# Kernel tuning notes

Measured on AMD Instinct MI355X. Metric: run time of the kernel, lower is better.

Reference implementation:

```python
import jax, jax.numpy as jnp
import numpy as np

EPS = 1e-3  # tfa InstanceNormalization default epsilon


def _inorm(x, g, b):
    # instance norm over the last two axes (the spatial extent of the attention map)
    mu = jnp.mean(x, axis=(-2, -1), keepdims=True)
    var = jnp.var(x, axis=(-2, -1), keepdims=True)
    return (x - mu) * jax.lax.rsqrt(var + EPS) * g + b


def setup_inputs() -> dict:
    key = jax.random.key(0)
    B, N, E, H = 4, 576, 256, 8
    C = 4 * E  # KV_size
    ks = jax.random.split(key, 24)

    def w(k, i, o):
        return jax.random.normal(k, (i, o), jnp.float32) * 0.02

    return {
        "emb1": jax.random.normal(ks[0], (B, N, E), jnp.float32),
        "emb2": jax.random.normal(ks[1], (B, N, E), jnp.float32),
        "emb3": jax.random.normal(ks[2], (B, N, E), jnp.float32),
        "emb4": jax.random.normal(ks[3], (B, N, E), jnp.float32),
        "emb_C": jax.random.normal(ks[4], (B, N, C), jnp.float32),
        "Wq_C": w(ks[5], C, C),
        "Wk_C": w(ks[6], C, C),
        "Wv_C": w(ks[7], C, C),
        "Wq1": w(ks[8], E, E),
        "Wq2": w(ks[9], E, E),
        "Wq3": w(ks[10], E, E),
        "Wq4": w(ks[11], E, E),
        "Wk": w(ks[12], E, E),
        "Wv": w(ks[13], E, E),
        "Wo1": w(ks[14], E, E),
        "Wo2": w(ks[15], E, E),
        "Wo3": w(ks[16], E, E),
        "Wo4": w(ks[17], E, E),
        "gamma1": jnp.ones((), jnp.float32),   # psi1 scale (channel axis has size 1)
        "beta1": jnp.zeros((), jnp.float32),
        "gamma2": jnp.ones((H,), jnp.float32),  # psi2 scale, channel axis = heads
        "beta2": jnp.zeros((H,), jnp.float32),
    }


def reference(emb1, emb2, emb3, emb4, emb_C, Wq_C, Wk_C, Wv_C,
              Wq1, Wq2, Wq3, Wq4, Wk, Wv, Wo1, Wo2, Wo3, Wo4,
              gamma1, beta1, gamma2, beta2):
    B, N, E = emb1.shape
    H = gamma2.shape[0]
    dh = E // H

    # ---- channel attention (inline InstanceNorm + softmax) ----
    QC = emb_C @ Wq_C  # (B,N,C)
    KC = emb_C @ Wk_C
    VC = emb_C @ Wv_C
    attn_c = jnp.einsum('bnc,bnd->bcd', QC, KC)                    # (B,C,C)
    sim_c = jax.nn.softmax(_inorm(attn_c, gamma1, beta1), axis=-1)
    T_hat = jnp.einsum('bcd,bnd->bnc', sim_c, VC)                  # (B,N,C)

    # split channel dim (C = 4E) into 4 chunks of E, concat along tokens -> (B,4N,E)
    KV_S = jnp.transpose(T_hat.reshape(B, N, 4, E), (0, 2, 1, 3)).reshape(B, 4 * N, E)

    def heads(x):  # (B,L,E) -> (B,H,L,dh)
        L = x.shape[1]
        return jnp.transpose(x.reshape(B, L, H, dh), (0, 2, 1, 3))

    # ---- 4-branch spatial multi-head attention with shared K/V ----
    Qs = jnp.stack([heads(emb1 @ Wq1), heads(emb2 @ Wq2),
                    heads(emb3 @ Wq3), heads(emb4 @ Wq4)])          # (4,B,H,N,dh)
    Kh = heads(KV_S @ Wk)                                           # (B,H,4N,dh)
    Vh = heads(KV_S @ Wv)

    attn = jnp.einsum('qbhnd,bhmd->qbhnm', Qs, Kh)                  # (4,B,H,N,4N)
    g = gamma2[:, None, None]
    b = beta2[:, None, None]
    sim = jax.nn.softmax(_inorm(attn, g, b), axis=-1)
    ctx = jnp.einsum('qbhnm,bhmd->qbhnd', sim, Vh)                  # (4,B,H,N,dh)
    ctx = jnp.transpose(ctx, (0, 1, 3, 2, 4)).reshape(4, B, N, E)

    return (ctx[0] @ Wo1, ctx[1] @ Wo2, ctx[2] @ Wo3, ctx[3] @ Wo4)
```

## Files before the change

### kernel.cpp

```cpp
#include <hip/hip_runtime.h>
#include <math.h>


namespace {
constexpr int Bq  = 4;
constexpr int Nn  = 576;
constexpr int Ee  = 256;
constexpr int Cc  = 1024;
constexpr int Mm  = 2304;
constexpr long BNE = (long)Bq * Nn * Ee;
constexpr long CCl = (long)Cc * Cc;
constexpr float EPSV = 1e-3f;
constexpr float LOG2E = 1.4426950408889634f;
}

typedef _Float16 h16;
typedef _Float16 h8v __attribute__((ext_vector_type(8)));
typedef _Float16 h4v __attribute__((ext_vector_type(4)));
typedef float    f4v __attribute__((ext_vector_type(4)));

struct WtP {
  const float* src[13]; h16* dst[13];
  const float* embC; h16* dEmbC;
};

__global__ __launch_bounds__(256) void wtrans(WtP p)
{
  const int bt = blockIdx.x;
  const int t = threadIdx.x;
  if (bt >= 928) {
    const long i4 = ((long)(bt - 928) * 256 + t) * 4;
    const float4 v = *(const float4*)(p.embC + i4);
    h4v o = {(h16)v.x, (h16)v.y, (h16)v.z, (h16)v.w};
    *(h4v*)(p.dEmbC + i4) = o;
    return;
  }
  __shared__ h16 Ls[64][64];
  int mi, tile, Kd, Nd;
  if (bt < 768) { mi = bt >> 8; tile = bt & 255; Kd = 1024; Nd = 1024; }
  else { const int r = bt - 768; mi = 3 + (r >> 4); tile = r & 15; Kd = 256; Nd = 256; }
  const int ntn = Nd >> 6;
  const int tk = tile / ntn, tn = tile % ntn;
  const float* src = p.src[mi] + (long)(tk * 64) * Nd + tn * 64;
  h16* dst = p.dst[mi] + (long)(tn * 64) * Kd + tk * 64;
  #pragma unroll
  for (int it = 0; it < 4; ++it) {
    const int kr = (t >> 4) + it * 16;
    const int c4 = (t & 15) * 4;
    const float4 v = *(const float4*)(src + (long)kr * Nd + c4);
    const float vv[4] = {v.x, v.y, v.z, v.w};
    #pragma unroll
    for (int jj = 0; jj < 4; ++jj) {
      const int n = c4 + jj;
      Ls[n][(((kr >> 3) ^ ((n >> 3) & 7)) << 3) | (kr & 7)] = (h16)vv[jj];
    }
  }
  __syncthreads();
  #pragma unroll
  for (int it = 0; it < 2; ++it) {
    const int n = t >> 2;
    const int k8 = (t & 3) + it * 4;
    const h8v o = *(const h8v*)&Ls[n][(k8 ^ ((n >> 3) & 7)) << 3];
    *(h8v*)(dst + (long)n * Kd + k8 * 8) = o;
  }
}

__global__ __launch_bounds__(256) void vtrans(
    const h16* __restrict__ V, h16* __restrict__ vT)
{
  __shared__ h16 Ls[32][64];
  const int kc = blockIdx.x;
  const int bh = blockIdx.y;
  const int b = bh >> 3, h = bh & 7;
  const int t = threadIdx.x;
  const int kv0 = kc * 64;
  {
    const int row = t >> 2, c8 = t & 3;
    const h8v v = *(const h8v*)(V + ((long)b * Mm + kv0 + row) * Ee + h * 32 + c8 * 8);
    #pragma unroll
    for (int e = 0; e < 8; ++e) {
      const int d = c8 * 8 + e;
      Ls[d][(((row >> 3) ^ ((d >> 3) & 7)) << 3) | (row & 7)] = v[e];
    }
  }
  __syncthreads();
  {
    const int d = t >> 3, j8 = t & 7;
    const h8v o = *(const h8v*)&Ls[d][(j8 ^ ((d >> 3) & 7)) << 3];
    *(h8v*)(vT + ((long)bh * 32 + d) * Mm + kv0 + j8 * 8) = o;
  }
}

struct GemmP {
  const h16* A[4]; const h16* B[4]; void* O[4][3]; const float* A32[4];
};

template <int BM, int TA, int TB, int AF32, int OUT16, int RM, int STATS, int OSHIFT>
__global__ __launch_bounds__(256) void mg(GemmP p, int K, int lda, int ldb,
                                          int ldc, float* stats)
{
  __shared__ h16 As[BM][64];
  __shared__ h16 Bs[128][64];
  const int z = blockIdx.z;
  const h16* A = p.A[z]; const h16* B = p.B[z]; const float* A32 = p.A32[z];
  const int n0 = blockIdx.x * 128, m0 = blockIdx.y * BM;
  const int t = threadIdx.x, w = t >> 6, lg = (t >> 4) & 3, lr = t & 15;
  constexpr int MF = 4, NF = (BM == 128 ? 4 : 2);
  const int wm = (BM == 128) ? (w & 1) * 64 : 0;
  const int wn = (BM == 128) ? (w >> 1) * 64 : w * 32;

  h8v   rA[AF32 ? 1 : BM / 32];
  float4 rF[AF32 ? BM / 16 : 1];
  h8v   rB[4];

  auto LOAD = [&](int kt) {
    if constexpr (AF32) {
      #pragma unroll
      for (int it = 0; it < BM / 16; ++it) {
        const int f = t + it * 256, row = f >> 4, c4 = f & 15;
        rF[it] = *(const float4*)(A32 + (long)(m0 + row) * lda + kt + c4 * 4);
      }
    } else if constexpr (TA == 0) {
      #pragma unroll
      for (int it = 0; it < BM / 32; ++it) {
        const int f = t + it * 256, row = f >> 3, c8 = f & 7;
        rA[it] = *(const h8v*)(A + (long)(m0 + row) * lda + kt + c8 * 8);
      }
    } else {
      #pragma unroll
      for (int it = 0; it < BM / 32; ++it) {
        const int f = t + it * 256;
        const int kr = (BM == 128) ? (f >> 4) : (f >> 3);
        const int mc = (BM == 128) ? (f & 15) : (f & 7);
        rA[it] = *(const h8v*)(A + (long)(kt + kr) * lda + m0 + mc * 8);
      }
    }
    if constexpr (TB == 0) {
      #pragma unroll
      for (int it = 0; it < 4; ++it) {
        const int f = t + it * 256, kr = f >> 4, nc = f & 15;
        rB[it] = *(const h8v*)(B + (long)(kt + kr) * ldb + n0 + nc * 8);
      }
    } else {
      #pragma unroll
      for (int it = 0; it < 4; ++it) {
        const int f = t + it * 256, row = f >> 3, c8 = f & 7;
        rB[it] = *(const h8v*)(B + (long)(n0 + row) * ldb + kt + c8 * 8);
      }
    }
  };

  auto STORE = [&]() {
    if constexpr (AF32) {
      #pragma unroll
      for (int it = 0; it < BM / 16; ++it) {
        const int f = t + it * 256, row = f >> 4, c4 = f & 15;
        const float4 v = rF[it];
        h4v o = {(h16)v.x, (h16)v.y, (h16)v.z, (h16)v.w};
        const int col = ((((c4 >> 1) ^ ((row >> 3) & 7)) << 3) | ((c4 & 1) << 2));
        *(h4v*)&As[row][col] = o;
      }
    } else if constexpr (TA == 0) {
      #pragma unroll
      for (int it = 0; it < BM / 32; ++it) {
        const int f = t + it * 256, row = f >> 3, c8 = f & 7;
        *(h8v*)&As[row][(c8 ^ ((row >> 3) & 7)) << 3] = rA[it];
      }
    } else {
      #pragma unroll
      for (int it = 0; it < BM / 32; ++it) {
        const int f = t + it * 256;
        const int kr = (BM == 128) ? (f >> 4) : (f >> 3);
        const int mc = (BM == 128) ? (f & 15) : (f & 7);
        const int colb = (((kr >> 3) ^ (mc & 7)) << 3) | (kr & 7);
        #pragma unroll
        for (int e = 0; e < 8; ++e) As[mc * 8 + e][colb] = rA[it][e];
      }
    }
    if constexpr (TB == 0) {
      #pragma unroll
      for (int it = 0; it < 4; ++it) {
        const int f = t + it * 256, kr = f >> 4, nc = f & 15;
        const int colb = (((kr >> 3) ^ (nc & 7)) << 3) | (kr & 7);
        #pragma unroll
        for (int e = 0; e < 8; ++e) Bs[nc * 8 + e][colb] = rB[it][e];
      }
    } else {
      #pragma unroll
      for (int it = 0; it < 4; ++it) {
        const int f = t + it * 256, row = f >> 3, c8 = f & 7;
        *(h8v*)&Bs[row][(c8 ^ ((row >> 3) & 7)) << 3] = rB[it];
      }
    }
  };

  f4v acc[MF][NF];
  #pragma unroll
  for (int i = 0; i < MF; ++i)
    #pragma unroll
    for (int j = 0; j < NF; ++j) acc[i][j] = (f4v){0.f, 0.f, 0.f, 0.f};

  LOAD(0);
  STORE();
  __syncthreads();

  for (int kt = 0;;) {
    const int ktn = kt + 64;
    const bool more = ktn < K;
    if (more) LOAD(ktn);

    #pragma unroll
    for (int ks = 0; ks < 2; ++ks) {
      h8v af[MF], bf[NF];
      #pragma unroll
      for (int mf = 0; mf < MF; ++mf) {
        const int row = wm + mf * 16 + lr;
        af[mf] = *(const h8v*)&As[row][((ks * 4 + lg) ^ ((row >> 3) & 7)) << 3];
      }
      #pragma unroll
      for (int nf = 0; nf < NF; ++nf) {
        const int row = wn + nf * 16 + lr;
        bf[nf] = *(const h8v*)&Bs[row][((ks * 4 + lg) ^ ((row >> 3) & 7)) << 3];
      }
      #pragma unroll
      for (int mf = 0; mf < MF; ++mf)
        #pragma unroll
        for (int nf = 0; nf < NF; ++nf)
          acc[mf][nf] = __builtin_amdgcn_mfma_f32_16x16x32_f16(af[mf], bf[nf], acc[mf][nf], 0, 0, 0);
    }
    if (!more) break;
    __syncthreads();
    STORE();
    __syncthreads();
    kt = ktn;
  }

  float s1 = 0.f, s2 = 0.f;
  #pragma unroll
  for (int mf = 0; mf < MF; ++mf)
    #pragma unroll
    for (int nf = 0; nf < NF; ++nf)
      #pragma unroll
      for (int r = 0; r < 4; ++r) {
        const int m = m0 + wm + mf * 16 + lg * 4 + r;
        const int n = n0 + wn + nf * 16 + lr;
        const float v = acc[mf][nf][r];
        if (STATS) { s1 += v; s2 += v * v; }
        if (RM) {
          ((h16*)p.O[z][0])[((long)(n >> 8) * Nn + m) * Ee + (n & 255)] = (h16)v;
        } else {
          const int chunk = n >> OSHIFT;
          const int col = n & ((1 << OSHIFT) - 1);
          if (OUT16) ((h16*)p.O[z][chunk])[(long)m * ldc + col] = (h16)v;
          else       ((float*)p.O[z][chunk])[(long)m * ldc + col] = v;
        }
      }
  if (STATS) {
    #pragma unroll
    for (int o = 1; o < 64; o <<= 1) { s1 += __shfl_xor(s1, o); s2 += __shfl_xor(s2, o); }
    if ((t & 63) == 0) { atomicAdd(&stats[z * 2], s1); atomicAdd(&stats[z * 2 + 1], s2); }
  }
}

__global__ __launch_bounds__(256) void softmax_c(
    const float* __restrict__ AC, const float* __restrict__ sums,
    const float* __restrict__ g1, h16* __restrict__ sim)
{
  __shared__ float red[256];
  const long r = blockIdx.x;
  const int b = (int)(r >> 10);
  const float* p = AC + r * Cc;
  const float invn = 1.f / (float)CCl;
  const float mean = sums[b * 2] * invn;
  const float var  = sums[b * 2 + 1] * invn - mean * mean;
  const float scb  = g1[0] * rsqrtf(var + EPSV);
  const int t = threadIdx.x;
  float4 v = ((const float4*)p)[t];
  v.x *= scb; v.y *= scb; v.z *= scb; v.w *= scb;
  float mx = fmaxf(fmaxf(v.x, v.y), fmaxf(v.z, v.w));
  red[t] = mx; __syncthreads();
  for (int s = 128; s > 0; s >>= 1) { if (t < s) red[t] = fmaxf(red[t], red[t + s]); __syncthreads(); }
  mx = red[0]; __syncthreads();
  v.x = __expf(v.x - mx); v.y = __expf(v.y - mx);
  v.z = __expf(v.z - mx); v.w = __expf(v.w - mx);
  red[t] = v.x + v.y + v.z + v.w; __syncthreads();
  for (int s = 128; s > 0; s >>= 1) { if (t < s) red[t] += red[t + s]; __syncthreads(); }
  const float inv = 1.f / red[0];
  h4v o = {(h16)(v.x * inv), (h16)(v.y * inv), (h16)(v.z * inv), (h16)(v.w * inv)};
  *(h4v*)&sim[r * Cc + t * 4] = o;
}

__global__ __launch_bounds__(256) void gram_all(
    const h16* __restrict__ Kb, const h16* __restrict__ Qb,
    float* __restrict__ Gk, float* __restrict__ km,
    float* __restrict__ Gq, float* __restrict__ qm)
{
  const int blk = blockIdx.x;
  const h16* slab; int ntiles; float* gout; float* msum;
  if (blk < 32) {
    slab = Kb + ((long)(blk >> 3) * Mm) * Ee + (blk & 7) * 32;
    ntiles = 12; gout = Gk + (long)blk * 1024; msum = km + blk * 32;
  } else {
    const int i = blk - 32, qq = i >> 5, b = (i >> 3) & 3, hd = i & 7;
    slab = Qb + (long)qq * BNE + ((long)b * Nn) * Ee + hd * 32;
    ntiles = 3; gout = Gq + (long)i * 1024; msum = qm + i * 32;
  }
  __shared__ float Ks[192][36];
  const int t = threadIdx.x;
  const int d = t >> 3, e0 = (t & 7) * 4;
  float g0 = 0.f, g1 = 0.f, g2 = 0.f, g3 = 0.f, cm = 0.f;
  for (int tile = 0; tile < ntiles; ++tile) {
    __syncthreads();
    #pragma unroll
    for (int it = 0; it < 3; ++it) {
      const int f = t + it * 256, row = f >> 2, c8 = f & 3;
      const h8v v = *(const h8v*)(slab + (long)(tile * 192 + row) * Ee + c8 * 8);
      #pragma unroll
      for (int e = 0; e < 8; ++e) Ks[row][c8 * 8 + e] = (float)v[e];
    }
    __syncthreads();
    #pragma unroll 4
    for (int m = 0; m < 192; ++m) {
      const float qd = Ks[m][d];
      const float4 qe = *(const float4*)&Ks[m][e0];
      g0 = fmaf(qd, qe.x, g0); g1 = fmaf(qd, qe.y, g1);
      g2 = fmaf(qd, qe.z, g2); g3 = fmaf(qd, qe.w, g3);
    }
    if (t < 32) {
      #pragma unroll 4
      for (int m = 0; m < 192; ++m) cm += Ks[m][t];
    }
  }
  float* gp = gout + d * 32 + e0;
  gp[0] = g0; gp[1] = g1; gp[2] = g2; gp[3] = g3;
  if (t < 32) msum[t] = cm;
}

__global__ __launch_bounds__(256) void finalize_scale2(
    const float* __restrict__ Gq, const float* __restrict__ Gk,
    const float* __restrict__ qm, const float* __restrict__ km,
    const float* __restrict__ g2, float* __restrict__ sc2)
{
  __shared__ float red[4];
  const int i = blockIdx.x;
  const int kb = i & 31;
  const int t = threadIdx.x;
  const float4 a = *(const float4*)(Gq + (long)i * 1024 + t * 4);
  const float4 b = *(const float4*)(Gk + (long)kb * 1024 + t * 4);
  float s = a.x * b.x + a.y * b.y + a.z * b.z + a.w * b.w;
  #pragma unroll
  for (int o = 1; o < 64; o <<= 1) s += __shfl_xor(s, o);
  if ((t & 63) == 0) red[t >> 6] = s;
  float mu = 0.f;
  if (t < 32) mu = qm[i * 32 + t] * km[kb * 32 + t];
  #pragma unroll
  for (int o = 1; o < 32; o <<= 1) mu += __shfl_xor(mu, o);
  __syncthreads();
  if (t == 0) {
    const float tot = red[0] + red[1] + red[2] + red[3];
    const float inv = 1.f / ((float)Nn * (float)Mm);
    const float ex2 = tot * inv;
    const float m1  = mu * inv;
    sc2[i] = g2[i & 7] * rsqrtf(ex2 - m1 * m1 + EPSV) * LOG2E;
  }
}

__global__ __launch_bounds__(256) void flash5(
    const h16* __restrict__ Qb, const h16* __restrict__ Kb,
    const h16* __restrict__ vT, const float* __restrict__ sc2,
    h16* __restrict__ ctx)
{
  __shared__ h16 Ks[128][40];
  __shared__ h16 Vt[32][136];
  __shared__ h16 Ps[64][136];
  const int pidx = blockIdx.x;
  const int x = pidx & 7, rest = pidx >> 3;
  const int j = rest % 36, g = rest / 36;
  const int bh = g * 8 + x, b = bh >> 3, hd = bh & 7;
  const int nt = j % 9, q = j / 9;
  const int t = threadIdx.x, w = t >> 6, lg = (t >> 4) & 3, lr = t & 15;
  const float sc = sc2[(q << 5) + bh];

  const h16* Qp = Qb + (long)q * BNE + (long)(b * Nn + nt * 64) * Ee + hd * 32;
  const h16* Kp = Kb + ((long)b * Mm) * Ee + hd * 32;
  const h16* Vp = vT + (long)bh * (32L * Mm);

  const h8v qf = *(const h8v*)(Qp + (long)(w * 16 + lr) * Ee + lg * 8);

  const int krow = t >> 1, kc = (t & 1) * 16;
  const int vd   = t >> 3, vc = (t & 7) * 16;

  h8v ka0, ka1, va0, va1;
  ka0 = *(const h8v*)(Kp + (long)krow * Ee + kc);
  ka1 = *(const h8v*)(Kp + (long)krow * Ee + kc + 8);
  va0 = *(const h8v*)(Vp + (long)vd * Mm + vc);
  va1 = *(const h8v*)(Vp + (long)vd * Mm + vc + 8);
  *(h8v*)&Ks[krow][kc]     = ka0;
  *(h8v*)&Ks[krow][kc + 8] = ka1;
  *(h8v*)&Vt[vd][vc]       = va0;
  *(h8v*)&Vt[vd][vc + 8]   = va1;

  float m_run = -3e38f, l_run = 0.f;
  f4v cacc[2];
  cacc[0] = (f4v){0.f, 0.f, 0.f, 0.f};
  cacc[1] = (f4v){0.f, 0.f, 0.f, 0.f};
  __syncthreads();

  for (int mt = 0; mt < 18; ++mt) {
    const bool more = mt < 17;
    if (more) {
      const long ko = (long)((mt + 1) * 128 + krow) * Ee + kc;
      ka0 = *(const h8v*)(Kp + ko);
      ka1 = *(const h8v*)(Kp + ko + 8);
      const long vo = (long)vd * Mm + (mt + 1) * 128 + vc;
      va0 = *(const h8v*)(Vp + vo);
      va1 = *(const h8v*)(Vp + vo + 8);
    }

    f4v s[8];
    #pragma unroll
    for (int nf = 0; nf < 8; ++nf) {
      const h8v kf = *(const h8v*)&Ks[nf * 16 + lr][lg * 8];
      s[nf] = __builtin_amdgcn_mfma_f32_16x16x32_f16(kf, qf, (f4v){0.f, 0.f, 0.f, 0.f}, 0, 0, 0);
    }
    float mx = -3e38f;
    #pragma unroll
    for (int nf = 0; nf < 8; ++nf)
      #pragma unroll
      for (int r = 0; r < 4; ++r) mx = fmaxf(mx, s[nf][r]);
    mx = fmaxf(mx, __shfl_xor(mx, 16));
    mx = fmaxf(mx, __shfl_xor(mx, 32));
    const float mnew = fmaxf(m_run, mx * sc);
    const float corr = __builtin_amdgcn_exp2f(m_run - mnew);
    float rs = 0.f;
    #pragma unroll
    for (int nf = 0; nf < 8; ++nf)
      #pragma unroll
      for (int r = 0; r < 4; ++r) {
        const float pv = __builtin_amdgcn_exp2f(fmaf(s[nf][r], sc, -mnew));
        s[nf][r] = pv; rs += pv;
      }
    rs += __shfl_xor(rs, 16);
    rs += __shfl_xor(rs, 32);
    l_run = l_run * corr + rs;
    m_run = mnew;
    #pragma unroll
    for (int r = 0; r < 4; ++r) {
      const float cr = __shfl(corr, lg * 4 + r);
      cacc[0][r] *= cr; cacc[1][r] *= cr;
    }
    #pragma unroll
    for (int nf = 0; nf < 8; ++nf) {
      h4v pk = {(h16)s[nf][0], (h16)s[nf][1], (h16)s[nf][2], (h16)s[nf][3]};
      *(h4v*)&Ps[w * 16 + lr][nf * 16 + lg * 4] = pk;
    }
    #pragma unroll
    for (int ks = 0; ks < 4; ++ks) {
      const h8v pf = *(const h8v*)&Ps[w * 16 + lr][ks * 32 + lg * 8];
      #pragma unroll
      for (int df = 0; df < 2; ++df) {
        const h8v vf = *(const h8v*)&Vt[df * 16 + lr][ks * 32 + lg * 8];
        cacc[df] = __builtin_amdgcn_mfma_f32_16x16x32_f16(pf, vf, cacc[df], 0, 0, 0);
      }
    }
    if (more) {
      __syncthreads();
      *(h8v*)&Ks[krow][kc]     = ka0;
      *(h8v*)&Ks[krow][kc + 8] = ka1;
      *(h8v*)&Vt[vd][vc]       = va0;
      *(h8v*)&Vt[vd][vc + 8]   = va1;
      __syncthreads();
    }
  }

  float linv[4];
  #pragma unroll
  for (int r = 0; r < 4; ++r) linv[r] = 1.f / __shfl(l_run, lg * 4 + r);
  h16* Op = ctx + (long)q * BNE + (long)(b * Nn + nt * 64) * Ee + hd * 32;
  #pragma unroll
  for (int r = 0; r < 4; ++r) {
    const long row = w * 16 + lg * 4 + r;
    Op[row * Ee + 0  + lr] = (h16)(cacc[0][r] * linv[r]);
    Op[row * Ee + 16 + lr] = (h16)(cacc[1][r] * linv[r]);
  }
}

extern "C" void kernel_launch(void* const* d_in, const int* in_sizes, int n_in,
                              void* d_out, int out_size, void* d_ws, size_t ws_size,
                              hipStream_t stream)
{
  (void)in_sizes; (void)n_in; (void)out_size; (void)ws_size;
  const float* emb[4] = {(const float*)d_in[0], (const float*)d_in[1],
                         (const float*)d_in[2], (const float*)d_in[3]};
  const float* gamma1 = (const float*)d_in[18];
  const float* gamma2 = (const float*)d_in[20];
  float* out = (float*)d_out;

  h16* hws = (h16*)d_ws;
  h16* embC16 = hws;
  h16* QC16   = hws + 2359296L;
  h16* KC16   = hws + 4718592L;
  h16* VC16   = hws + 7077888L;
  h16* attnR  = hws + 9437184L;
  float* attnC = (float*)attnR;
  h16* WcT  = hws + 17825792L;
  h16* WkvT = WcT + 3145728L;
  h16* WqT  = WkvT + 131072L;
  h16* WoT  = WqT + 262144L;
  float* stats = (float*)(hws + 21626880L);
  float* sums = stats;
  float* Gk   = stats + 8;
  float* km   = Gk + 32768;
  float* Gq   = km + 1024;
  float* qm   = Gq + 131072;
  float* sc2v = qm + 4096;
  h16* sim16  = QC16;
  h16* KVS16  = embC16;
  h16* Kbuf16 = attnR;
  h16* Vbuf16 = attnR + 2359296L;
  h16* Qbuf16 = attnR + 4718592L;
  h16* vT     = embC16;
  h16* ctx16  = VC16;

  hipMemsetAsync(sums, 0, 8 * sizeof(float), stream);

  {
    WtP wp;
    wp.src[0] = (const float*)d_in[5];  wp.dst[0] = WcT;
    wp.src[1] = (const float*)d_in[6];  wp.dst[1] = WcT + 1048576L;
    wp.src[2] = (const float*)d_in[7];  wp.dst[2] = WcT + 2097152L;
    wp.src[3] = (const float*)d_in[12]; wp.dst[3] = WkvT;
    wp.src[4] = (const float*)d_in[13]; wp.dst[4] = WkvT + 65536L;
    for (int i = 0; i < 4; ++i) {
      wp.src[5 + i] = (const float*)d_in[8 + i];  wp.dst[5 + i] = WqT + (long)i * 65536;
      wp.src[9 + i] = (const float*)d_in[14 + i]; wp.dst[9 + i] = WoT + (long)i * 65536;
    }
    wp.embC = (const float*)d_in[4]; wp.dEmbC = embC16;
    wtrans<<<3232, 256, 0, stream>>>(wp);
  }

  {
    GemmP gp{};
    gp.A[0] = embC16; gp.B[0] = WcT;
    gp.O[0][0] = QC16; gp.O[0][1] = KC16; gp.O[0][2] = VC16;
    mg<64,0,1,0,1,0,0,10><<<dim3(24,36,1), 256, 0, stream>>>(gp, 1024, 1024, 1024, 1024, nullptr);
  }
  {
    GemmP gp{};
    for (int z = 0; z < 4; ++z) {
      gp.A[z] = QC16 + (long)z * 589824; gp.B[z] = KC16 + (long)z * 589824;
      gp.O[z][0] = attnC + (long)z * CCl;
    }
    mg<64,1,0,0,0,0,1,30><<<dim3(8,16,4), 256, 0, stream>>>(gp, 576, 1024, 1024, 1024, sums);
  }
  softmax_c<<<4096, 256, 0, stream>>>(attnC, sums, gamma1, sim16);
  {
    GemmP gp{};
    for (int z = 0; z < 4; ++z) {
      gp.A[z] = VC16 + (long)z * 589824; gp.B[z] = sim16 + (long)z * CCl;
      gp.O[z][0] = KVS16 + (long)z * 589824;
    }
    mg<64,0,1,0,1,1,0,30><<<dim3(8,9,4), 256, 0, stream>>>(gp, 1024, 1024, 1024, 256, nullptr);
  }
  {
    GemmP gp{};
    gp.A[0] = KVS16; gp.B[0] = WkvT;
    gp.O[0][0] = Kbuf16; gp.O[0][1] = Vbuf16;
    mg<64,0,1,0,1,0,0,8><<<dim3(4,144,1), 256, 0, stream>>>(gp, 256, 256, 256, 256, nullptr);
  }
  {
    GemmP gp{};
    for (int z = 0; z < 4; ++z) {
      gp.A32[z] = emb[z]; gp.B[z] = WqT + (long)z * 65536;
      gp.O[z][0] = Qbuf16 + (long)z * 589824;
    }
    mg<64,0,1,1,1,0,0,30><<<dim3(2,36,4), 256, 0, stream>>>(gp, 256, 256, 256, 256, nullptr);
  }
  vtrans<<<dim3(36,32), 256, 0, stream>>>(Vbuf16, vT);
  gram_all<<<160, 256, 0, stream>>>(Kbuf16, Qbuf16, Gk, km, Gq, qm);
  finalize_scale2<<<128, 256, 0, stream>>>(Gq, Gk, qm, km, gamma2, sc2v);
  flash5<<<1152, 256, 0, stream>>>(Qbuf16, Kbuf16, vT, sc2v, ctx16);
  {
    GemmP gp{};
    for (int z = 0; z < 4; ++z) {
      gp.A[z] = ctx16 + (long)z * 589824; gp.B[z] = WoT + (long)z * 65536;
      gp.O[z][0] = out + (long)z * 589824;
    }
    mg<64,0,1,0,0,0,0,30><<<dim3(2,36,4), 256, 0, stream>>>(gp, 256, 256, 256, 256, nullptr);
  }
}
```

Before: 427.3 us.

## Compute Gram matrices with MFMA and split K slabs across blocks

Replaces the scalar-FMA LDS-tiled Gram kernel with an MFMA 16x16x32 f16 version that loads rows straight from global memory into fragments. Four waves each accumulate a partial result, which is reduced through shared memory. Each K slab is split across two blocks that combine their results with atomicAdd, which adds parallelism. The memset is widened to zero the K Gram and column-sum buffers. The cost is strided scalar half-precision global loads and atomic contention, with fp32 accumulation kept.

```diff
diff --git a/kernel.cpp b/kernel.cpp
--- a/kernel.cpp
+++ b/kernel.cpp
@@ -290,50 +290,82 @@
   *(h4v*)&sim[r * Cc + t * 4] = o;
 }
 
-__global__ __launch_bounds__(256) void gram_all(
+__global__ __launch_bounds__(256) void gram2(
     const h16* __restrict__ Kb, const h16* __restrict__ Qb,
     float* __restrict__ Gk, float* __restrict__ km,
     float* __restrict__ Gq, float* __restrict__ qm)
 {
+  __shared__ float Gw[4][1024];
+  __shared__ float csw[4][32];
   const int blk = blockIdx.x;
-  const h16* slab; int ntiles; float* gout; float* msum;
-  if (blk < 32) {
-    slab = Kb + ((long)(blk >> 3) * Mm) * Ee + (blk & 7) * 32;
-    ntiles = 12; gout = Gk + (long)blk * 1024; msum = km + blk * 32;
+  const int t = threadIdx.x, w = t >> 6, lg = (t >> 4) & 3, lr = t & 15;
+
+  const h16* slab; float* gout; float* msum;
+  int nsteps; bool katomic;
+  if (blk < 64) {
+    const int bh = blk >> 1, chunk = blk & 1;
+    slab = Kb + ((long)(bh >> 3) * Mm + chunk * 1152) * Ee + (bh & 7) * 32;
+    gout = Gk + (long)bh * 1024; msum = km + bh * 32;
+    nsteps = 36; katomic = true;
   } else {
-    const int i = blk - 32, qq = i >> 5, b = (i >> 3) & 3, hd = i & 7;
+    const int i = blk - 64, qq = i >> 5, b = (i >> 3) & 3, hd = i & 7;
     slab = Qb + (long)qq * BNE + ((long)b * Nn) * Ee + hd * 32;
-    ntiles = 3; gout = Gq + (long)i * 1024; msum = qm + i * 32;
-  }
-  __shared__ float Ks[192][36];
-  const int t = threadIdx.x;
-  const int d = t >> 3, e0 = (t & 7) * 4;
-  float g0 = 0.f, g1 = 0.f, g2 = 0.f, g3 = 0.f, cm = 0.f;
-  for (int tile = 0; tile < ntiles; ++tile) {
-    __syncthreads();
-    #pragma unroll
-    for (int it = 0; it < 3; ++it) {
-      const int f = t + it * 256, row = f >> 2, c8 = f & 3;
-      const h8v v = *(const h8v*)(slab + (long)(tile * 192 + row) * Ee + c8 * 8);
-      #pragma unroll
-      for (int e = 0; e < 8; ++e) Ks[row][c8 * 8 + e] = (float)v[e];
-    }
-    __syncthreads();
-    #pragma unroll 4
-    for (int m = 0; m < 192; ++m) {
-      const float qd = Ks[m][d];
-      const float4 qe = *(const float4*)&Ks[m][e0];
-      g0 = fmaf(qd, qe.x, g0); g1 = fmaf(qd, qe.y, g1);
-      g2 = fmaf(qd, qe.z, g2); g3 = fmaf(qd, qe.w, g3);
-    }
-    if (t < 32) {
-      #pragma unroll 4
-      for (int m = 0; m < 192; ++m) cm += Ks[m][t];
-    }
-  }
-  float* gp = gout + d * 32 + e0;
-  gp[0] = g0; gp[1] = g1; gp[2] = g2; gp[3] = g3;
-  if (t < 32) msum[t] = cm;
+    gout = Gq + (long)i * 1024; msum = qm + i * 32;
+    nsteps = 18; katomic = false;
+  }
+
+  f4v acc[2][2];
+  #pragma unroll
+  for (int i = 0; i < 2; ++i)
+    #pragma unroll
+    for (int j = 0; j < 2; ++j) acc[i][j] = (f4v){0.f, 0.f, 0.f, 0.f};
+  float cs0 = 0.f, cs1 = 0.f;
+
+  for (int s = w; s < nsteps; s += 4) {
+    const long rbase = (long)s * 32 + lg * 8;
+    h8v f0, f1;
+    #pragma unroll
+    for (int j = 0; j < 8; ++j) {
+      const h16* rp = slab + (rbase + j) * Ee;
+      f0[j] = rp[lr];
+      f1[j] = rp[lr + 16];
+      cs0 += (float)f0[j];
+      cs1 += (float)f1[j];
+    }
+    acc[0][0] = __builtin_amdgcn_mfma_f32_16x16x32_f16(f0, f0, acc[0][0], 0, 0, 0);
+    acc[0][1] = __builtin_amdgcn_mfma_f32_16x16x32_f16(f0, f1, acc[0][1], 0, 0, 0);
+    acc[1][0] = __builtin_amdgcn_mfma_f32_16x16x32_f16(f1, f0, acc[1][0], 0, 0, 0);
+    acc[1][1] = __builtin_amdgcn_mfma_f32_16x16x32_f16(f1, f1, acc[1][1], 0, 0, 0);
+  }
+
+  cs0 += __shfl_xor(cs0, 16); cs0 += __shfl_xor(cs0, 32);
+  cs1 += __shfl_xor(cs1, 16); cs1 += __shfl_xor(cs1, 32);
+  if (lg == 0) { csw[w][lr] = cs0; csw[w][lr + 16] = cs1; }
+
+  #pragma unroll
+  for (int i = 0; i < 2; ++i)
+    #pragma unroll
+    for (int j = 0; j < 2; ++j)
+      #pragma unroll
+      for (int r = 0; r < 4; ++r) {
+        const int d = i * 16 + lg * 4 + r;
+        const int e = j * 16 + lr;
+        Gw[w][d * 32 + e] = acc[i][j][r];
+      }
+  __syncthreads();
+
+  #pragma unroll
+  for (int u = 0; u < 4; ++u) {
+    const int flat = t + u * 256;
+    const float v = Gw[0][flat] + Gw[1][flat] + Gw[2][flat] + Gw[3][flat];
+    if (katomic) atomicAdd(&gout[flat], v);
+    else gout[flat] = v;
+  }
+  if (t < 32) {
+    const float m = csw[0][t] + csw[1][t] + csw[2][t] + csw[3][t];
+    if (katomic) atomicAdd(&msum[t], m);
+    else msum[t] = m;
+  }
 }
 
 __global__ __launch_bounds__(256) void finalize_scale2(
@@ -522,7 +554,7 @@
   h16* vT     = embC16;
   h16* ctx16  = VC16;
 
-  hipMemsetAsync(sums, 0, 8 * sizeof(float), stream);
+  hipMemsetAsync(sums, 0, (8 + 32768 + 1024) * sizeof(float), stream);
 
   {
     WtP wp;
@@ -577,7 +609,7 @@
     mg<64,0,1,1,1,0,0,30><<<dim3(2,36,4), 256, 0, stream>>>(gp, 256, 256, 256, 256, nullptr);
   }
   vtrans<<<dim3(36,32), 256, 0, stream>>>(Vbuf16, vT);
-  gram_all<<<160, 256, 0, stream>>>(Kbuf16, Qbuf16, Gk, km, Gq, qm);
+  gram2<<<192, 256, 0, stream>>>(Kbuf16, Qbuf16, Gk, km, Gq, qm);
   finalize_scale2<<<128, 256, 0, stream>>>(Gq, Gk, qm, km, gamma2, sc2v);
   flash5<<<1152, 256, 0, stream>>>(Qbuf16, Kbuf16, vT, sc2v, ctx16);
   {
```

Result: faster. 354.9 us (-16.9%).
